# Kernel optimization log

Measured on AMD Instinct MI355X. Metric: run time of the kernel, lower is better.

Reference implementation:

```python
import jax, jax.numpy as jnp
import numpy as np

SOBEL_X = jnp.array([[-1., 0., 1.], [-2., 0., 2.], [-1., 0., 1.]], dtype=jnp.float32).reshape(1, 1, 3, 3)
SOBEL_Y = jnp.array([[-1., -2., -1.], [0., 0., 0.], [1., 2., 1.]], dtype=jnp.float32).reshape(1, 1, 3, 3)
KERNEL_MASK = jnp.ones((1, 1, 3, 3), dtype=jnp.float32)


def _conv(x, k):
    # x: (N,1,H,W), k: (1,1,3,3), SAME padding (matches torch padding=1)
    return jax.lax.conv_general_dilated(
        x, k, window_strides=(1, 1), padding='SAME',
        dimension_numbers=('NCHW', 'OIHW', 'NCHW'))


def setup_inputs() -> dict:
    key = jax.random.key(0)
    k1, k2, k3 = jax.random.split(key, 3)
    shape = (2, 6, 512, 512, 8)  # (B, T, H, W, F)
    prediction = jax.random.normal(k1, shape, dtype=jnp.float32)
    target = jax.random.normal(k2, shape, dtype=jnp.float32)
    mask = jax.random.randint(k3, shape, 0, 2, dtype=jnp.int32)
    return {"prediction": prediction, "target": target, "mask": mask}


def reference(prediction, target, mask):
    B, T, H, W, F = prediction.shape
    # (B,T,H,W,F) -> (B*T*F, 1, H, W)
    def to_nchw(x):
        return x.transpose(0, 1, 4, 2, 3).reshape(B * T * F, 1, H, W)

    mask_r = to_nchw(mask.astype(jnp.float32))
    pred_r = to_nchw(prediction)
    tgt_r = to_nchw(target)

    valid = (_conv(mask_r, KERNEL_MASK) == 9.0).astype(prediction.dtype)

    gx_p = _conv(pred_r, SOBEL_X) * valid
    gy_p = _conv(pred_r, SOBEL_Y) * valid
    gx_t = _conv(tgt_r, SOBEL_X) * valid
    gy_t = _conv(tgt_r, SOBEL_Y) * valid

    # mode == 'l1'
    loss = jnp.abs(gx_p - gx_t) + jnp.abs(gy_p - gy_t)
    # (B*T*F,1,H,W) -> (B,T,H,W,F)
    return loss.reshape(B, T, F, H, W).transpose(0, 1, 3, 4, 2)
```

## Files before the change

### kernel.cpp

```cpp
#include <hip/hip_runtime.h>


constexpr int H = 512;
constexpr int W = 512;
constexpr int F = 8;
constexpr int IMAGES = 12;
constexpr int ROWSTRIDE = W * F;
constexpr int TILES_PER_IMG = (H / 16) * (W / 16);

__global__ __launch_bounds__(256) void sobel_loss_kernel(
    const float* __restrict__ pred,
    const float* __restrict__ tgt,
    const int*   __restrict__ mask,
    float*       __restrict__ out)
{
    const int tid = threadIdx.x;
    const int tw  = tid & 15;
    const int th  = tid >> 4;

    int bid = blockIdx.x;
    const int img  = bid / TILES_PER_IMG;
    const int tile = bid - img * TILES_PER_IMG;
    const int h = ((tile >> 5) << 4) + th;
    const int w = ((tile & 31) << 4) + tw;

    const int pos = img * (H * W * F) + (h * W + w) * F;

    if (h == 0 || h == H - 1 || w == 0 || w == W - 1) {
        *(float4*)(out + pos)     = make_float4(0.f, 0.f, 0.f, 0.f);
        *(float4*)(out + pos + 4) = make_float4(0.f, 0.f, 0.f, 0.f);
        return;
    }

#pragma unroll
    for (int q = 0; q < 2; ++q) {
        const int p0 = pos + q * 4;

        float4 d[3][3];
        int4 mv = make_int4(1, 1, 1, 1);

#pragma unroll
        for (int i = 0; i < 3; ++i) {
#pragma unroll
            for (int j = 0; j < 3; ++j) {
                const int o = p0 + (i - 1) * ROWSTRIDE + (j - 1) * F;
                const float4 p = *(const float4*)(pred + o);
                const float4 t = *(const float4*)(tgt + o);
                d[i][j] = make_float4(p.x - t.x, p.y - t.y, p.z - t.z, p.w - t.w);
                const int4 m = *(const int4*)(mask + o);
                mv.x &= m.x; mv.y &= m.y; mv.z &= m.z; mv.w &= m.w;
            }
        }

        float4 r;
#define SOBEL_COMP(c)                                                          \
        {                                                                      \
            float gx = (d[0][2].c - d[0][0].c)                                 \
                     + 2.f * (d[1][2].c - d[1][0].c)                           \
                     + (d[2][2].c - d[2][0].c);                                \
            float gy = (d[2][0].c - d[0][0].c)                                 \
                     + 2.f * (d[2][1].c - d[0][1].c)                           \
                     + (d[2][2].c - d[0][2].c);                                \
            r.c = (mv.c != 0) ? (fabsf(gx) + fabsf(gy)) : 0.f;                 \
        }
        SOBEL_COMP(x)
        SOBEL_COMP(y)
        SOBEL_COMP(z)
        SOBEL_COMP(w)
#undef SOBEL_COMP

        *(float4*)(out + p0) = r;
    }
}

extern "C" void kernel_launch(void* const* d_in, const int* in_sizes, int n_in,
                              void* d_out, int out_size, void* d_ws, size_t ws_size,
                              hipStream_t stream) {
    const float* pred = (const float*)d_in[0];
    const float* tgt  = (const float*)d_in[1];
    const int*   mask = (const int*)d_in[2];
    float*       out  = (float*)d_out;

    const int blocks = IMAGES * TILES_PER_IMG;
    sobel_loss_kernel<<<blocks, 256, 0, stream>>>(pred, tgt, mask, out);
}
```

Before: 364.2 us.

## Stage pred-target differences and packed mask bits in LDS tiles

Each block now loads a 16x32-pixel tile plus halo into shared memory. The loader stores the pred-minus-target difference as float4 and packs the eight per-feature mask bits into one unsigned per pixel. The stencil then reads its nine neighbours from LDS instead of issuing nine redundant global loads per pixel per input, which cuts global traffic to roughly one pass over each input. Border pixels are handled because out-of-range mask bits are zero, at the cost of a barrier and about 40KB of LDS per block, which may limit occupancy.

Result: faster. 302.9 us (-16.8%).

```diff
diff --git a/kernel.cpp b/kernel.cpp
--- a/kernel.cpp
+++ b/kernel.cpp
@@ -5,8 +5,12 @@
 constexpr int W = 512;
 constexpr int F = 8;
 constexpr int IMAGES = 12;
-constexpr int ROWSTRIDE = W * F;
-constexpr int TILES_PER_IMG = (H / 16) * (W / 16);
+constexpr int TH = 16;
+constexpr int TWP = 32;
+constexpr int SR = TH + 2;
+constexpr int SP = TWP + 2;
+constexpr int SU = SP * 2;
+constexpr int TILES_PER_IMG = (H / TH) * (W / TWP);
 
 __global__ __launch_bounds__(256) void sobel_loss_kernel(
     const float* __restrict__ pred,
@@ -14,62 +18,95 @@
     const int*   __restrict__ mask,
     float*       __restrict__ out)
 {
+    __shared__ float4   sd[SR * SU];
+    __shared__ unsigned sm[SR * SP];
+
     const int tid = threadIdx.x;
-    const int tw  = tid & 15;
-    const int th  = tid >> 4;
+    const int img  = blockIdx.x >> 9;
+    const int tile = blockIdx.x & 511;
+    const int h0 = (tile >> 4) << 4;
+    const int w0 = (tile & 15) << 5;
+    const size_t ibase = (size_t)img * (H * W * F);
 
-    int bid = blockIdx.x;
-    const int img  = bid / TILES_PER_IMG;
-    const int tile = bid - img * TILES_PER_IMG;
-    const int h = ((tile >> 5) << 4) + th;
-    const int w = ((tile & 31) << 4) + tw;
-
-    const int pos = img * (H * W * F) + (h * W + w) * F;
-
-    if (h == 0 || h == H - 1 || w == 0 || w == W - 1) {
-        *(float4*)(out + pos)     = make_float4(0.f, 0.f, 0.f, 0.f);
-        *(float4*)(out + pos + 4) = make_float4(0.f, 0.f, 0.f, 0.f);
-        return;
+#pragma unroll
+    for (int it = 0; it < 5; ++it) {
+        const int s = tid + it * 256;
+        if (s < SR * SU) {
+            const int row = s / SU;
+            const int u   = s - row * SU;
+            const int gh  = h0 - 1 + row;
+            const int gp  = w0 - 1 + (u >> 1);
+            const int q   = u & 1;
+            const int ghc = min(max(gh, 0), H - 1);
+            const int gpc = min(max(gp, 0), W - 1);
+            const size_t off = ibase + ((size_t)ghc * W + gpc) * F + q * 4;
+            const float4 p = *(const float4*)(pred + off);
+            const float4 t = *(const float4*)(tgt + off);
+            sd[s] = make_float4(p.x - t.x, p.y - t.y, p.z - t.z, p.w - t.w);
+        }
     }
 
 #pragma unroll
-    for (int q = 0; q < 2; ++q) {
-        const int p0 = pos + q * 4;
+    for (int it = 0; it < 3; ++it) {
+        const int s = tid + it * 256;
+        if (s < SR * SP) {
+            const int row = s / SP;
+            const int px  = s - row * SP;
+            const int gh  = h0 - 1 + row;
+            const int gp  = w0 - 1 + px;
+            unsigned b = 0u;
+            if (gh >= 0 && gh < H && gp >= 0 && gp < W) {
+                const int* mp = mask + ibase + ((size_t)gh * W + gp) * F;
+                const int4 m0 = *(const int4*)mp;
+                const int4 m1 = *(const int4*)(mp + 4);
+                b = (unsigned)(m0.x | (m0.y << 1) | (m0.z << 2) | (m0.w << 3) |
+                               (m1.x << 4) | (m1.y << 5) | (m1.z << 6) | (m1.w << 7));
+            }
+            sm[s] = b;
+        }
+    }
+
+    __syncthreads();
+
+#pragma unroll
+    for (int it = 0; it < 4; ++it) {
+        const int o   = tid + it * 256;
+        const int row = o >> 6;
+        const int u   = o & 63;
+        const int c   = u >> 1;
+        const int q   = u & 1;
 
         float4 d[3][3];
-        int4 mv = make_int4(1, 1, 1, 1);
-
+        unsigned vm = 0xFFu;
 #pragma unroll
-        for (int i = 0; i < 3; ++i) {
+        for (int dy = 0; dy < 3; ++dy) {
 #pragma unroll
-            for (int j = 0; j < 3; ++j) {
-                const int o = p0 + (i - 1) * ROWSTRIDE + (j - 1) * F;
-                const float4 p = *(const float4*)(pred + o);
-                const float4 t = *(const float4*)(tgt + o);
-                d[i][j] = make_float4(p.x - t.x, p.y - t.y, p.z - t.z, p.w - t.w);
-                const int4 m = *(const int4*)(mask + o);
-                mv.x &= m.x; mv.y &= m.y; mv.z &= m.z; mv.w &= m.w;
+            for (int dx = 0; dx < 3; ++dx) {
+                d[dy][dx] = sd[(row + dy) * SU + (c + dx) * 2 + q];
+                vm &= sm[(row + dy) * SP + (c + dx)];
             }
         }
+        const unsigned vq = vm >> (q * 4);
 
         float4 r;
-#define SOBEL_COMP(c)                                                          \
+#define SOBEL_COMP(comp, bit)                                                  \
         {                                                                      \
-            float gx = (d[0][2].c - d[0][0].c)                                 \
-                     + 2.f * (d[1][2].c - d[1][0].c)                           \
-                     + (d[2][2].c - d[2][0].c);                                \
-            float gy = (d[2][0].c - d[0][0].c)                                 \
-                     + 2.f * (d[2][1].c - d[0][1].c)                           \
-                     + (d[2][2].c - d[0][2].c);                                \
-            r.c = (mv.c != 0) ? (fabsf(gx) + fabsf(gy)) : 0.f;                 \
+            float gx = (d[0][2].comp - d[0][0].comp)                           \
+                     + 2.f * (d[1][2].comp - d[1][0].comp)                     \
+                     + (d[2][2].comp - d[2][0].comp);                          \
+            float gy = (d[2][0].comp - d[0][0].comp)                           \
+                     + 2.f * (d[2][1].comp - d[0][1].comp)                     \
+                     + (d[2][2].comp - d[0][2].comp);                          \
+            r.comp = (vq & (1u << bit)) ? (fabsf(gx) + fabsf(gy)) : 0.f;       \
         }
-        SOBEL_COMP(x)
-        SOBEL_COMP(y)
-        SOBEL_COMP(z)
-        SOBEL_COMP(w)
+        SOBEL_COMP(x, 0)
+        SOBEL_COMP(y, 1)
+        SOBEL_COMP(z, 2)
+        SOBEL_COMP(w, 3)
 #undef SOBEL_COMP
 
-        *(float4*)(out + p0) = r;
+        const size_t off = ibase + ((size_t)(h0 + row) * W + (w0 + c)) * F + q * 4;
+        *(float4*)(out + off) = r;
     }
 }
 
```

## Stream rows with register sliding window and shared-memory separable Sobel

Applied to the files above, without the earlier changes.

Each block now handles a 128-pixel-wide strip over 16 rows and walks down the rows. Each thread keeps three rows of pred-minus-target differences and packed mask bits in registers, so every row is loaded once instead of nine times per output. Vertical partial sums go through double-buffered shared memory, with one barrier per row, to finish the horizontal part of the separable Sobel. This cuts redundant global loads and L2 traffic, but adds a sequential row loop, a barrier each row, and halo loads done by only four threads.

Result: faster. 319.6 us (-12.3%).

```diff
diff --git a/kernel.cpp b/kernel.cpp
--- a/kernel.cpp
+++ b/kernel.cpp
@@ -1,12 +1,42 @@
 #include <hip/hip_runtime.h>
 
 
-constexpr int H = 512;
-constexpr int W = 512;
-constexpr int F = 8;
+constexpr int H = 512, W = 512, F = 8;
 constexpr int IMAGES = 12;
-constexpr int ROWSTRIDE = W * F;
-constexpr int TILES_PER_IMG = (H / 16) * (W / 16);
+constexpr int TILE_W = 128;
+constexpr int SEG_H  = 16;
+constexpr int SUN    = (TILE_W + 2) * 2;
+constexpr int STRIPS = W / TILE_W;
+constexpr int SEGS   = H / SEG_H;
+constexpr size_t IMG_ELEMS = (size_t)H * W * F;
+
+__device__ __forceinline__ void lgkm_barrier() {
+    asm volatile("s_waitcnt lgkmcnt(0)\n\ts_barrier" ::: "memory");
+}
+
+__device__ __forceinline__ float4 sub4(float4 a, float4 b) {
+    return make_float4(a.x - b.x, a.y - b.y, a.z - b.z, a.w - b.w);
+}
+
+__device__ __forceinline__ unsigned packm(int4 m, bool in) {
+    unsigned pk = (unsigned)(m.x | (m.y << 1) | (m.z << 2) | (m.w << 3));
+    return in ? pk : 0u;
+}
+
+__device__ __forceinline__ void load_raw(const float* __restrict__ pred,
+                                         const float* __restrict__ tgt,
+                                         const int*   __restrict__ mask,
+                                         size_t ibase, int h, int gp, int q,
+                                         float4& p, float4& t, int4& m, bool& in)
+{
+    in = (h >= 0) & (h < H) & (gp >= 0) & (gp < W);
+    const int hc  = min(max(h, 0), H - 1);
+    const int gpc = min(max(gp, 0), W - 1);
+    const size_t off = ibase + ((size_t)hc * W + gpc) * F + q * 4;
+    p = *(const float4*)(pred + off);
+    t = *(const float4*)(tgt + off);
+    m = *(const int4*)(mask + off);
+}
 
 __global__ __launch_bounds__(256) void sobel_loss_kernel(
     const float* __restrict__ pred,
@@ -14,62 +44,85 @@
     const int*   __restrict__ mask,
     float*       __restrict__ out)
 {
+    __shared__ float4   sv1[2][SUN];
+    __shared__ float4   sv2[2][SUN];
+    __shared__ unsigned smv[2][SUN];
+
     const int tid = threadIdx.x;
-    const int tw  = tid & 15;
-    const int th  = tid >> 4;
+    const int q   = tid & 1;
+    const int pl  = tid >> 1;
+    const int bid = blockIdx.x;
+    const int img   = bid >> 7;
+    const int r     = bid & 127;
+    const int strip = r >> 5;
+    const int seg   = r & 31;
+    const int w0 = strip * TILE_W;
+    const int h0 = seg * SEG_H;
+    const size_t ibase = (size_t)img * IMG_ELEMS;
+    const int gp = w0 - 1 + pl;
 
-    int bid = blockIdx.x;
-    const int img  = bid / TILES_PER_IMG;
-    const int tile = bid - img * TILES_PER_IMG;
-    const int h = ((tile >> 5) << 4) + th;
-    const int w = ((tile & 31) << 4) + tw;
-
-    const int pos = img * (H * W * F) + (h * W + w) * F;
-
-    if (h == 0 || h == H - 1 || w == 0 || w == W - 1) {
-        *(float4*)(out + pos)     = make_float4(0.f, 0.f, 0.f, 0.f);
-        *(float4*)(out + pos + 4) = make_float4(0.f, 0.f, 0.f, 0.f);
-        return;
+    float4 dm1, d0c, dp1;
+    unsigned mm1, m0c, mp1;
+    {
+        float4 p, t; int4 m; bool in;
+        load_raw(pred, tgt, mask, ibase, h0 - 1, gp, q, p, t, m, in);
+        dm1 = sub4(p, t); mm1 = packm(m, in);
+        load_raw(pred, tgt, mask, ibase, h0,     gp, q, p, t, m, in);
+        d0c = sub4(p, t); m0c = packm(m, in);
+        load_raw(pred, tgt, mask, ibase, h0 + 1, gp, q, p, t, m, in);
+        dp1 = sub4(p, t); mp1 = packm(m, in);
     }
 
-#pragma unroll
-    for (int q = 0; q < 2; ++q) {
-        const int p0 = pos + q * 4;
+    for (int h = h0; h < h0 + SEG_H; ++h) {
+        float4 pn, tn; int4 mn4; bool inn;
+        load_raw(pred, tgt, mask, ibase, h + 2, gp, q, pn, tn, mn4, inn);
 
-        float4 d[3][3];
-        int4 mv = make_int4(1, 1, 1, 1);
+        const int s = h & 1;
 
-#pragma unroll
-        for (int i = 0; i < 3; ++i) {
-#pragma unroll
-            for (int j = 0; j < 3; ++j) {
-                const int o = p0 + (i - 1) * ROWSTRIDE + (j - 1) * F;
-                const float4 p = *(const float4*)(pred + o);
-                const float4 t = *(const float4*)(tgt + o);
-                d[i][j] = make_float4(p.x - t.x, p.y - t.y, p.z - t.z, p.w - t.w);
-                const int4 m = *(const int4*)(mask + o);
-                mv.x &= m.x; mv.y &= m.y; mv.z &= m.z; mv.w &= m.w;
-            }
+        if (tid < 4) {
+            const int hq  = tid & 1;
+            const int hgp = w0 + 127 + (tid >> 1);
+            float4 pa, ta, pb, tb, pc, tc; int4 ma4, mb4, mc4; bool ia, ib, ic;
+            load_raw(pred, tgt, mask, ibase, h - 1, hgp, hq, pa, ta, ma4, ia);
+            load_raw(pred, tgt, mask, ibase, h,     hgp, hq, pb, tb, mb4, ib);
+            load_raw(pred, tgt, mask, ibase, h + 1, hgp, hq, pc, tc, mc4, ic);
+            const float4 a = sub4(pa, ta), b = sub4(pb, tb), c = sub4(pc, tc);
+            sv1[s][256 + tid] = make_float4(a.x + 2.f * b.x + c.x,
+                                            a.y + 2.f * b.y + c.y,
+                                            a.z + 2.f * b.z + c.z,
+                                            a.w + 2.f * b.w + c.w);
+            sv2[s][256 + tid] = sub4(c, a);
+            smv[s][256 + tid] = packm(ma4, ia) & packm(mb4, ib) & packm(mc4, ic);
         }
 
-        float4 r;
-#define SOBEL_COMP(c)                                                          \
-        {                                                                      \
-            float gx = (d[0][2].c - d[0][0].c)                                 \
-                     + 2.f * (d[1][2].c - d[1][0].c)                           \
-                     + (d[2][2].c - d[2][0].c);                                \
-            float gy = (d[2][0].c - d[0][0].c)                                 \
-                     + 2.f * (d[2][1].c - d[0][1].c)                           \
-                     + (d[2][2].c - d[0][2].c);                                \
-            r.c = (mv.c != 0) ? (fabsf(gx) + fabsf(gy)) : 0.f;                 \
-        }
-        SOBEL_COMP(x)
-        SOBEL_COMP(y)
-        SOBEL_COMP(z)
-        SOBEL_COMP(w)
-#undef SOBEL_COMP
+        const float4 v1 = make_float4(dm1.x + 2.f * d0c.x + dp1.x,
+                                      dm1.y + 2.f * d0c.y + dp1.y,
+                                      dm1.z + 2.f * d0c.z + dp1.z,
+                                      dm1.w + 2.f * d0c.w + dp1.w);
+        const float4 v2 = sub4(dp1, dm1);
+        const unsigned mv = mm1 & m0c & mp1;
+        sv1[s][tid] = v1;
+        sv2[s][tid] = v2;
+        smv[s][tid] = mv;
 
-        *(float4*)(out + p0) = r;
+        lgkm_barrier();
+
+        const float4 v1r = sv1[s][tid + 4];
+        const float4 v2m = sv2[s][tid + 2];
+        const float4 v2r = sv2[s][tid + 4];
+        const unsigned valid = mv & smv[s][tid + 2] & smv[s][tid + 4];
+
+        float4 res;
+        res.x = (valid & 1u) ? fabsf(v1r.x - v1.x) + fabsf(v2.x + 2.f * v2m.x + v2r.x) : 0.f;
+        res.y = (valid & 2u) ? fabsf(v1r.y - v1.y) + fabsf(v2.y + 2.f * v2m.y + v2r.y) : 0.f;
+        res.z = (valid & 4u) ? fabsf(v1r.z - v1.z) + fabsf(v2.z + 2.f * v2m.z + v2r.z) : 0.f;
+        res.w = (valid & 8u) ? fabsf(v1r.w - v1.w) + fabsf(v2.w + 2.f * v2m.w + v2r.w) : 0.f;
+
+        *(float4*)(out + ibase + ((size_t)h * W + (w0 + pl)) * F + q * 4) = res;
+
+        dm1 = d0c; mm1 = m0c;
+        d0c = dp1; m0c = mp1;
+        dp1 = sub4(pn, tn); mp1 = packm(mn4, inn);
     }
 }
 
@@ -81,6 +134,6 @@
     const int*   mask = (const int*)d_in[2];
     float*       out  = (float*)d_out;
 
-    const int blocks = IMAGES * TILES_PER_IMG;
+    const int blocks = IMAGES * STRIPS * SEGS;
     sobel_loss_kernel<<<blocks, 256, 0, stream>>>(pred, tgt, mask, out);
 }
```

## Stream rows per wavefront with register sliding window and shuffles for columns

Applied to the files above, without the earlier changes.

Each wavefront now owns a 32-pixel-wide column strip (30 output columns plus halo) and walks down a 32-row segment. It keeps three rows of pred-minus-target differences and packed mask bits in registers, and prefetches two rows ahead. The separable Sobel is computed with vertical sums in registers and horizontal neighbours fetched via cross-lane shuffles. This replaces the nine-tap reload of each pixel and is meant to cut the redundant L2/global traffic of the old 16x16 tile scheme. In exchange it adds halo overlap between strips, shuffle overhead, a serial per-wavefront loop, and a boundary mask check that changes how edge pixels are zeroed.

New measurement: 326.3 us. -10.4%, faster.

```diff
diff --git a/kernel.cpp b/kernel.cpp
--- a/kernel.cpp
+++ b/kernel.cpp
@@ -1,12 +1,48 @@
 #include <hip/hip_runtime.h>
 
 
-constexpr int H = 512;
-constexpr int W = 512;
-constexpr int F = 8;
+constexpr int H = 512, W = 512, F = 8;
 constexpr int IMAGES = 12;
-constexpr int ROWSTRIDE = W * F;
-constexpr int TILES_PER_IMG = (H / 16) * (W / 16);
+constexpr int SEG_H = 32;
+constexpr int SEGS = H / SEG_H;
+constexpr int STRIPS = 18;
+constexpr int ROWE = W * F;
+constexpr size_t IMG_ELEMS = (size_t)H * W * F;
+
+__device__ __forceinline__ float4 sub4(float4 a, float4 b) {
+    return make_float4(a.x - b.x, a.y - b.y, a.z - b.z, a.w - b.w);
+}
+
+__device__ __forceinline__ float4 shfl4(float4 v, int src) {
+    float4 r;
+    r.x = __shfl(v.x, src, 64);
+    r.y = __shfl(v.y, src, 64);
+    r.z = __shfl(v.z, src, 64);
+    r.w = __shfl(v.w, src, 64);
+    return r;
+}
+
+struct RowRaw { float4 p, t; int4 m; };
+
+__device__ __forceinline__ RowRaw load_row(const float* __restrict__ pred,
+                                           const float* __restrict__ tgt,
+                                           const int*   __restrict__ mask,
+                                           size_t colbase, int h) {
+    const int hc = min(max(h, 0), H - 1);
+    const size_t off = colbase + (size_t)hc * ROWE;
+    RowRaw r;
+    r.p = *(const float4*)(pred + off);
+    r.t = *(const float4*)(tgt + off);
+    r.m = *(const int4*)(mask + off);
+    return r;
+}
+
+__device__ __forceinline__ void fold(const RowRaw& r, int hval, bool gpin,
+                                     float4& d, unsigned& mv) {
+    d = sub4(r.p, r.t);
+    const unsigned pk = (unsigned)(r.m.x | (r.m.y << 1) | (r.m.z << 2) | (r.m.w << 3));
+    mv = (hval >= 0 && hval < H && gpin) ? pk : 0u;
+}
 
 __global__ __launch_bounds__(256) void sobel_loss_kernel(
     const float* __restrict__ pred,
@@ -14,62 +50,74 @@
     const int*   __restrict__ mask,
     float*       __restrict__ out)
 {
-    const int tid = threadIdx.x;
-    const int tw  = tid & 15;
-    const int th  = tid >> 4;
+    const int lane = threadIdx.x & 63;
+    const int wid  = (blockIdx.x << 2) + (threadIdx.x >> 6);
+    const int seg  = wid & (SEGS - 1);
+    const int t2   = wid >> 4;
+    const int strip = t2 % STRIPS;
+    const int img   = t2 / STRIPS;
 
-    int bid = blockIdx.x;
-    const int img  = bid / TILES_PER_IMG;
-    const int tile = bid - img * TILES_PER_IMG;
-    const int h = ((tile >> 5) << 4) + th;
-    const int w = ((tile & 31) << 4) + tw;
+    const int h0 = seg << 5;
+    const int ws = strip * 30;
+    const int p  = lane >> 1;
+    const int qq = lane & 1;
+    const int gp = ws - 1 + p;
+    const bool gpin = (gp >= 0) & (gp < W);
+    const int gpc = min(max(gp, 0), W - 1);
+    const size_t ibase = (size_t)img * IMG_ELEMS;
+    const size_t colbase = ibase + (size_t)gpc * F + qq * 4;
 
-    const int pos = img * (H * W * F) + (h * W + w) * F;
+    float4 dm1, d0c, dp1;
+    unsigned mm1, m0c, mp1;
+    {
+        RowRaw r = load_row(pred, tgt, mask, colbase, h0 - 1);
+        fold(r, h0 - 1, gpin, dm1, mm1);
+        r = load_row(pred, tgt, mask, colbase, h0);
+        fold(r, h0, gpin, d0c, m0c);
+        r = load_row(pred, tgt, mask, colbase, h0 + 1);
+        fold(r, h0 + 1, gpin, dp1, mp1);
+    }
+    RowRaw stageA = load_row(pred, tgt, mask, colbase, h0 + 2);
+    RowRaw stageB = load_row(pred, tgt, mask, colbase, h0 + 3);
 
-    if (h == 0 || h == H - 1 || w == 0 || w == W - 1) {
-        *(float4*)(out + pos)     = make_float4(0.f, 0.f, 0.f, 0.f);
-        *(float4*)(out + pos + 4) = make_float4(0.f, 0.f, 0.f, 0.f);
-        return;
-    }
+    const bool do_store = (p >= 1) & (p < 31) & (gp < W);
+    const int lm2 = lane - 2, lp2 = lane + 2;
+    const int hmax = h0 + SEG_H;
 
-#pragma unroll
-    for (int q = 0; q < 2; ++q) {
-        const int p0 = pos + q * 4;
+    float* const outcol = out + ibase + (size_t)gp * F + qq * 4;
 
-        float4 d[3][3];
-        int4 mv = make_int4(1, 1, 1, 1);
+    auto step = [&](int h, RowRaw& stage) {
+        const float4 v1 = make_float4(fmaf(2.f, d0c.x, dm1.x) + dp1.x,
+                                      fmaf(2.f, d0c.y, dm1.y) + dp1.y,
+                                      fmaf(2.f, d0c.z, dm1.z) + dp1.z,
+                                      fmaf(2.f, d0c.w, dm1.w) + dp1.w);
+        const float4 v2 = sub4(dp1, dm1);
+        const unsigned mvv = mm1 & m0c & mp1;
 
-#pragma unroll
-        for (int i = 0; i < 3; ++i) {
-#pragma unroll
-            for (int j = 0; j < 3; ++j) {
-                const int o = p0 + (i - 1) * ROWSTRIDE + (j - 1) * F;
-                const float4 p = *(const float4*)(pred + o);
-                const float4 t = *(const float4*)(tgt + o);
-                d[i][j] = make_float4(p.x - t.x, p.y - t.y, p.z - t.z, p.w - t.w);
-                const int4 m = *(const int4*)(mask + o);
-                mv.x &= m.x; mv.y &= m.y; mv.z &= m.z; mv.w &= m.w;
-            }
-        }
+        const float4 v1l = shfl4(v1, lm2), v1r = shfl4(v1, lp2);
+        const float4 v2l = shfl4(v2, lm2), v2r = shfl4(v2, lp2);
+        const unsigned ml = (unsigned)__shfl((int)mvv, lm2, 64);
+        const unsigned mr = (unsigned)__shfl((int)mvv, lp2, 64);
+        const unsigned valid = mvv & ml & mr;
 
-        float4 r;
-#define SOBEL_COMP(c)                                                          \
-        {                                                                      \
-            float gx = (d[0][2].c - d[0][0].c)                                 \
-                     + 2.f * (d[1][2].c - d[1][0].c)                           \
-                     + (d[2][2].c - d[2][0].c);                                \
-            float gy = (d[2][0].c - d[0][0].c)                                 \
-                     + 2.f * (d[2][1].c - d[0][1].c)                           \
-                     + (d[2][2].c - d[0][2].c);                                \
-            r.c = (mv.c != 0) ? (fabsf(gx) + fabsf(gy)) : 0.f;                 \
-        }
-        SOBEL_COMP(x)
-        SOBEL_COMP(y)
-        SOBEL_COMP(z)
-        SOBEL_COMP(w)
-#undef SOBEL_COMP
+        float4 res;
+        res.x = (valid & 1u) ? fabsf(v1r.x - v1l.x) + fabsf(fmaf(2.f, v2.x, v2l.x) + v2r.x) : 0.f;
+        res.y = (valid & 2u) ? fabsf(v1r.y - v1l.y) + fabsf(fmaf(2.f, v2.y, v2l.y) + v2r.y) : 0.f;
+        res.z = (valid & 4u) ? fabsf(v1r.z - v1l.z) + fabsf(fmaf(2.f, v2.z, v2l.z) + v2r.z) : 0.f;
+        res.w = (valid & 8u) ? fabsf(v1r.w - v1l.w) + fabsf(fmaf(2.f, v2.w, v2l.w) + v2r.w) : 0.f;
 
-        *(float4*)(out + p0) = r;
+        if (do_store)
+            *(float4*)(outcol + (size_t)h * ROWE) = res;
+
+        dm1 = d0c; mm1 = m0c;
+        d0c = dp1; m0c = mp1;
+        fold(stage, h + 2, gpin, dp1, mp1);
+        stage = load_row(pred, tgt, mask, colbase, min(h + 4, hmax));
+    };
+
+    for (int h = h0; h < hmax; h += 2) {
+        step(h,     stageA);
+        step(h + 1, stageB);
     }
 }
 
@@ -81,6 +129,6 @@
     const int*   mask = (const int*)d_in[2];
     float*       out  = (float*)d_out;
 
-    const int blocks = IMAGES * TILES_PER_IMG;
+    const int blocks = IMAGES * STRIPS * SEGS / 4;
     sobel_loss_kernel<<<blocks, 256, 0, stream>>>(pred, tgt, mask, out);
 }
```
